# Kernel tuning notes

Measured on AMD Instinct MI355X. Metric: run time of the kernel, lower is better.

The kernel has to match this reference:

```python
import jax, jax.numpy as jnp
import numpy as np

N = 100_000      # nodes
E = 1_200_000    # edges (avg degree 12)
F_IN = 6         # node_features
H = 64           # hidden_channels
L = 3            # num_layers
EPS = 1e-5       # BatchNorm eps


def setup_inputs() -> dict:
    key = jax.random.key(0)
    ks = jax.random.split(key, 16)
    s = 0.1
    return {
        "x": jax.random.normal(ks[0], (N, F_IN), jnp.float32),
        "edge_index": jax.random.randint(ks[1], (2, E), 0, N, dtype=jnp.int32),
        "edge_attr": jax.random.uniform(ks[2], (E, 1), jnp.float32),
        # node encoder
        "W_enc": jax.random.normal(ks[3], (F_IN, H), jnp.float32) * s,
        "b_enc": jnp.zeros((H,), jnp.float32),
        # per-layer GNN params (stacked over L layers)
        "W_edge": jax.random.normal(ks[4], (L, 1, H), jnp.float32) * s,
        "b_edge": jnp.zeros((L, H), jnp.float32),
        "W_upd": jax.random.normal(ks[5], (L, 2 * H, H), jnp.float32) * s,
        "b_upd": jnp.zeros((L, H), jnp.float32),
        # batch norm (eval mode: running stats)
        "bn_gamma": jnp.ones((L, H), jnp.float32),
        "bn_beta": jnp.zeros((L, H), jnp.float32),
        "bn_mean": jnp.zeros((L, H), jnp.float32),
        "bn_var": jnp.ones((L, H), jnp.float32),
        # path predictor MLP
        "W_p1": jax.random.normal(ks[6], (H, H), jnp.float32) * s,
        "b_p1": jnp.zeros((H,), jnp.float32),
        "W_p2": jax.random.normal(ks[7], (H, 1), jnp.float32) * s,
        "b_p2": jnp.zeros((1,), jnp.float32),
    }


def reference(x, edge_index, edge_attr, W_enc, b_enc, W_edge, b_edge,
              W_upd, b_upd, bn_gamma, bn_beta, bn_mean, bn_var,
              W_p1, b_p1, W_p2, b_p2):
    src, dst = edge_index[0], edge_index[1]  # PyG source_to_target flow
    h = x @ W_enc + b_enc                    # [N, H]
    for i in range(L):
        # message: x_j * lin_edge(edge_attr)
        edge_feat = edge_attr @ W_edge[i] + b_edge[i]      # [E, H]
        msg = h[src] * edge_feat                           # gather + multiply
        # aggregate: scatter-max to target nodes; PyG fills empty rows with 0
        agg = jax.ops.segment_max(msg, dst, num_segments=N)
        agg = jnp.where(jnp.isfinite(agg), agg, 0.0)
        # update: relu(lin_update(cat[x, aggr]))
        h = jax.nn.relu(jnp.concatenate([h, agg], axis=1) @ W_upd[i] + b_upd[i])
        # BatchNorm1d (eval) + relu  (dropout p=0.1 is identity at inference)
        h = (h - bn_mean[i]) * (bn_gamma[i] / jnp.sqrt(bn_var[i] + EPS)) + bn_beta[i]
        h = jax.nn.relu(h)
    # path predictor: Linear -> ReLU -> Linear
    path_scores = jax.nn.relu(h @ W_p1 + b_p1) @ W_p2 + b_p2  # [N, 1]
    return path_scores
```

## Files before the change

### kernel.cpp

```cpp
#include <hip/hip_runtime.h>
#include <hip/hip_fp16.h>

#define FIN 6
#define HC 64
#define LAYERS 3
#define CAP 64

typedef _Float16 f16x8 __attribute__((ext_vector_type(8)));
typedef float f32x4 __attribute__((ext_vector_type(4)));

__global__ void PathfindingGNN_17274358464713_kernel() {}

__global__ __launch_bounds__(256) void k_enc_scatter(const float* __restrict__ x,
                                                     const float* __restrict__ Wenc,
                                                     const float* __restrict__ benc,
                                                     __half* __restrict__ h16,
                                                     int Nn,
                                                     const int* __restrict__ src,
                                                     const int* __restrict__ dst,
                                                     const float* __restrict__ ea,
                                                     int* __restrict__ counts,
                                                     unsigned int* __restrict__ bucket,
                                                     int E, int edgeB) {
  if ((int)blockIdx.x < edgeB) {
    int e = blockIdx.x * 256 + threadIdx.x;
    if (e < E) {
      int d = dst[e];
      int p = atomicAdd(&counts[d], 1);
      if (p < CAP) {
        unsigned int q = (unsigned int)(ea[e] * 32767.0f + 0.5f);
        bucket[d * CAP + p] = (unsigned int)src[e] | (q << 17);
      }
    }
    return;
  }
  int idx = (blockIdx.x - edgeB) * 256 + threadIdx.x;
  if (idx >= Nn * HC) return;
  int n = idx >> 6, c = idx & 63;
  float s = benc[c];
#pragma unroll
  for (int f = 0; f < FIN; ++f)
    s = fmaf(x[n * FIN + f], Wenc[f * HC + c], s);
  h16[idx] = __float2half(s);
}

__global__ __launch_bounds__(256, 6) void k_layer(const __half* __restrict__ h16,
                                                  const int* __restrict__ counts,
                                                  const unsigned int* __restrict__ bucket,
                                                  const float* __restrict__ We, const float* __restrict__ be,
                                                  const float* __restrict__ W, const float* __restrict__ b,
                                                  const float* __restrict__ gam, const float* __restrict__ bet,
                                                  const float* __restrict__ mean, const float* __restrict__ var,
                                                  __half* __restrict__ out16, int Nn,
                                                  int last, const float* __restrict__ Wp1,
                                                  const float* __restrict__ bp1, const float* __restrict__ Wp2,
                                                  const float* __restrict__ bp2, float* __restrict__ pred) {
  __shared__ alignas(16) __half Wt[64][136];
  __shared__ alignas(16) __half Asm[64][72];

  const int tid = threadIdx.x;
  const int nb = blockIdx.x * 64;
  const int w = tid >> 6;
  const float inv15 = 1.0f / 32767.0f;

  for (int i = tid; i < 128 * 64; i += 256) {
    int k = i >> 6, col = i & 63;
    Wt[col][k] = __float2half(W[i]);
  }

  {
    const int lhw = tid & 31;
    const int hw = (tid >> 5) & 1;
    const int ch0 = lhw * 2;
    const float2 wev = *(const float2*)&We[ch0];
    const float2 bev = *(const float2*)&be[ch0];
    for (int i = 0; i < 8; ++i) {
      int nl = w * 16 + i + 8 * hw;
      int nc = min(nb + nl, Nn - 1);
      int r = nc * CAP;
      int r1 = r + min(counts[nc], CAP);
      float m0 = -INFINITY, m1 = -INFINITY;
#define PROC(vv) {                                                                     \
      unsigned int v_ = (vv);                                                          \
      float qf = (float)(v_ >> 17) * inv15;                                            \
      float2 hf = __half22float2(*(const __half2*)&h16[(v_ & 0x1FFFFu) * HC + ch0]);   \
      m0 = fmaxf(m0, hf.x * fmaf(qf, wev.x, bev.x));                                   \
      m1 = fmaxf(m1, hf.y * fmaf(qf, wev.y, bev.y)); }
      for (; r + 8 <= r1; r += 8) {
        uint4 va = *(const uint4*)&bucket[r];
        uint4 vb = *(const uint4*)&bucket[r + 4];
        PROC(va.x) PROC(va.y) PROC(va.z) PROC(va.w)
        PROC(vb.x) PROC(vb.y) PROC(vb.z) PROC(vb.w)
      }
      if (r + 4 <= r1) {
        uint4 va = *(const uint4*)&bucket[r];
        PROC(va.x) PROC(va.y) PROC(va.z) PROC(va.w)
        r += 4;
      }
      for (; r < r1; ++r) { PROC(bucket[r]) }
#undef PROC
      float o0 = (m0 == -INFINITY) ? 0.0f : m0;
      float o1 = (m1 == -INFINITY) ? 0.0f : m1;
      *(__half2*)&Asm[nl][ch0] = __floats2half2_rn(o0, o1);
    }
  }
  __syncthreads();

  const int lr = tid & 15;
  const int lg = (tid >> 4) & 3;
  f32x4 acc[4];
#pragma unroll
  for (int t = 0; t < 4; ++t) acc[t] = (f32x4){0.f, 0.f, 0.f, 0.f};
  const int arow = min(nb + w * 16 + lr, Nn - 1);
#pragma unroll
  for (int kc = 0; kc < 4; ++kc) {
    const int kof = kc * 32 + lg * 8;
    f16x8 a;
    if (kc < 2)
      a = *(const f16x8*)&h16[arow * HC + kof];
    else
      a = *(const f16x8*)&Asm[w * 16 + lr][kof - 64];
#pragma unroll
    for (int t = 0; t < 4; ++t) {
      f16x8 bf = *(const f16x8*)&Wt[t * 16 + lr][kof];
      acc[t] = __builtin_amdgcn_mfma_f32_16x16x32_f16(a, bf, acc[t], 0, 0, 0);
    }
  }

  float o[4][4];
#pragma unroll
  for (int t = 0; t < 4; ++t) {
    int cc = t * 16 + lr;
    float bias = b[cc];
    float sc = gam[cc] * rsqrtf(var[cc] + 1e-5f);
    float sh = bet[cc] - mean[cc] * sc;
#pragma unroll
    for (int r = 0; r < 4; ++r) {
      float v = fmaxf(acc[t][r] + bias, 0.f);
      o[t][r] = fmaxf(fmaf(v, sc, sh), 0.f);
    }
  }

  const int rbase = nb + w * 16 + lg * 4;
  if (!last) {
#pragma unroll
    for (int r = 0; r < 4; ++r) {
      int n = rbase + r;
      if (n < Nn) {
#pragma unroll
        for (int t = 0; t < 4; ++t)
          out16[n * HC + t * 16 + lr] = __float2half(o[t][r]);
      }
    }
    return;
  }

  __syncthreads();
#pragma unroll
  for (int t = 0; t < 4; ++t)
#pragma unroll
    for (int r = 0; r < 4; ++r)
      Asm[w * 16 + lg * 4 + r][t * 16 + lr] = __float2half(o[t][r]);
  for (int i = tid; i < 64 * 64; i += 256) {
    int k = i >> 6, col = i & 63;
    Wt[col][k] = __float2half(Wp1[i]);
  }
  __syncthreads();

  f32x4 acc2[4];
#pragma unroll
  for (int t = 0; t < 4; ++t) acc2[t] = (f32x4){0.f, 0.f, 0.f, 0.f};
#pragma unroll
  for (int kc = 0; kc < 2; ++kc) {
    const int kof = kc * 32 + lg * 8;
    f16x8 a = *(const f16x8*)&Asm[w * 16 + lr][kof];
#pragma unroll
    for (int t = 0; t < 4; ++t) {
      f16x8 bf = *(const f16x8*)&Wt[t * 16 + lr][kof];
      acc2[t] = __builtin_amdgcn_mfma_f32_16x16x32_f16(a, bf, acc2[t], 0, 0, 0);
    }
  }

  float s[4] = {0.f, 0.f, 0.f, 0.f};
#pragma unroll
  for (int t = 0; t < 4; ++t) {
    int cc = t * 16 + lr;
    float b1 = bp1[cc], w2 = Wp2[cc];
#pragma unroll
    for (int r = 0; r < 4; ++r) {
      float pv = fmaxf(acc2[t][r] + b1, 0.f);
      s[r] = fmaf(pv, w2, s[r]);
    }
  }
#pragma unroll
  for (int msk = 1; msk < 16; msk <<= 1) {
#pragma unroll
    for (int r = 0; r < 4; ++r) s[r] += __shfl_xor(s[r], msk, 64);
  }
  if (lr == 0) {
    float b2 = bp2[0];
#pragma unroll
    for (int r = 0; r < 4; ++r) {
      int n = rbase + r;
      if (n < Nn) pred[n] = s[r] + b2;
    }
  }
}

extern "C" void kernel_launch(void* const* d_in, const int* in_sizes, int n_in,
                              void* d_out, int out_size, void* d_ws, size_t ws_size,
                              hipStream_t stream) {
  const float* x = (const float*)d_in[0];
  const int* eidx = (const int*)d_in[1];
  const float* eattr = (const float*)d_in[2];
  const float* Wenc = (const float*)d_in[3];
  const float* benc = (const float*)d_in[4];
  const float* Wedge = (const float*)d_in[5];
  const float* bedge = (const float*)d_in[6];
  const float* Wupd = (const float*)d_in[7];
  const float* bupd = (const float*)d_in[8];
  const float* bng = (const float*)d_in[9];
  const float* bnb = (const float*)d_in[10];
  const float* bnm = (const float*)d_in[11];
  const float* bnv = (const float*)d_in[12];
  const float* Wp1 = (const float*)d_in[13];
  const float* bp1 = (const float*)d_in[14];
  const float* Wp2 = (const float*)d_in[15];
  const float* bp2 = (const float*)d_in[16];

  const int Nn = in_sizes[0] / FIN;
  const int E = in_sizes[1] / 2;
  const int* src = eidx;
  const int* dst = eidx + E;
  const int NH = Nn * HC;

  size_t off = 0;
  char* base = (char*)d_ws;
  auto carve = [&](size_t bytes) -> void* {
    void* p = base + off;
    off += (bytes + 255) & ~(size_t)255;
    return p;
  };
  int* counts = (int*)carve((size_t)Nn * 4);
  unsigned int* bucket = (unsigned int*)carve((size_t)Nn * CAP * 4);
  __half* hA16 = (__half*)carve((size_t)NH * 2);
  __half* hB16 = (__half*)carve((size_t)NH * 2);
  if (off > ws_size) return;

  int nhB = (NH + 255) / 256;
  int edgeB = (E + 255) / 256;
  int updB = (Nn + 63) / 64;

  hipMemsetAsync(counts, 0, (size_t)Nn * 4, stream);
  k_enc_scatter<<<edgeB + nhB, 256, 0, stream>>>(x, Wenc, benc, hA16, Nn,
                                                 src, dst, eattr, counts, bucket, E, edgeB);

  __half* hc16 = hA16;
  __half* hn16 = hB16;
  for (int i = 0; i < LAYERS; ++i) {
    int last = (i == LAYERS - 1) ? 1 : 0;
    k_layer<<<updB, 256, 0, stream>>>(hc16, counts, bucket,
                                      Wedge + i * HC, bedge + i * HC,
                                      Wupd + i * 2 * HC * HC, bupd + i * HC,
                                      bng + i * HC, bnb + i * HC, bnm + i * HC, bnv + i * HC,
                                      hn16, Nn,
                                      last, Wp1, bp1, Wp2, bp2, (float*)d_out);
    __half* t16 = hc16; hc16 = hn16; hn16 = t16;
  }
}
```

Baseline: 365.4 us.

## Prefetch edge buckets with nontemporal loads and vectorize encoder writes

Bucket records are now written and read with nontemporal hints, so edge lists streamed once per layer do not evict the reused node features from cache. The gather loop software-prefetches the first four records of the next node while the current one is processed. Per-node counts are loaded once per wave and broadcast with shuffles. The encoder computes two channels per thread with half2 stores. The cost is more branching in the aggregation loop and a narrower unrolled body (4 records instead of 8 per step), which may reduce memory-level parallelism for high-degree nodes.

```diff
diff --git a/kernel.cpp b/kernel.cpp
--- a/kernel.cpp
+++ b/kernel.cpp
@@ -8,6 +8,11 @@
 
 typedef _Float16 f16x8 __attribute__((ext_vector_type(8)));
 typedef float f32x4 __attribute__((ext_vector_type(4)));
+typedef unsigned int u32x4 __attribute__((ext_vector_type(4)));
+
+__device__ inline u32x4 ntload4(const unsigned int* p) {
+  return __builtin_nontemporal_load(reinterpret_cast<const u32x4*>(p));
+}
 
 __global__ void PathfindingGNN_17274358464713_kernel() {}
 
@@ -29,19 +34,24 @@
       int p = atomicAdd(&counts[d], 1);
       if (p < CAP) {
         unsigned int q = (unsigned int)(ea[e] * 32767.0f + 0.5f);
-        bucket[d * CAP + p] = (unsigned int)src[e] | (q << 17);
+        unsigned int rec = (unsigned int)src[e] | (q << 17);
+        __builtin_nontemporal_store(rec, &bucket[d * CAP + p]);
       }
     }
     return;
   }
   int idx = (blockIdx.x - edgeB) * 256 + threadIdx.x;
-  if (idx >= Nn * HC) return;
-  int n = idx >> 6, c = idx & 63;
-  float s = benc[c];
-#pragma unroll
-  for (int f = 0; f < FIN; ++f)
-    s = fmaf(x[n * FIN + f], Wenc[f * HC + c], s);
-  h16[idx] = __float2half(s);
+  if (idx >= Nn * (HC / 2)) return;
+  int n = idx >> 5, cp = (idx & 31) * 2;
+  float s0 = benc[cp], s1 = benc[cp + 1];
+#pragma unroll
+  for (int f = 0; f < FIN; ++f) {
+    float xv = x[n * FIN + f];
+    float2 wv = *(const float2*)&Wenc[f * HC + cp];
+    s0 = fmaf(xv, wv.x, s0);
+    s1 = fmaf(xv, wv.y, s1);
+  }
+  *(__half2*)&h16[n * HC + cp] = __floats2half2_rn(s0, s1);
 }
 
 __global__ __launch_bounds__(256, 6) void k_layer(const __half* __restrict__ h16,
@@ -74,11 +84,19 @@
     const int ch0 = lhw * 2;
     const float2 wev = *(const float2*)&We[ch0];
     const float2 bev = *(const float2*)&be[ch0];
+    int ldn = min(nb + w * 16 + (tid & 15), Nn - 1);
+    int ldc = min(counts[ldn], CAP);
+    auto rof = [&](int i) {
+      return min(nb + w * 16 + i + 8 * hw, Nn - 1) * CAP;
+    };
+    u32x4 pf = ntload4(&bucket[rof(0)]);
     for (int i = 0; i < 8; ++i) {
       int nl = w * 16 + i + 8 * hw;
-      int nc = min(nb + nl, Nn - 1);
-      int r = nc * CAP;
-      int r1 = r + min(counts[nc], CAP);
+      int cnt = __shfl(ldc, i + 8 * hw, 64);
+      int r0 = rof(i);
+      int r1 = r0 + cnt;
+      u32x4 cur = pf;
+      if (i < 7) pf = ntload4(&bucket[rof(i + 1)]);
       float m0 = -INFINITY, m1 = -INFINITY;
 #define PROC(vv) {                                                                     \
       unsigned int v_ = (vv);                                                          \
@@ -86,18 +104,21 @@
       float2 hf = __half22float2(*(const __half2*)&h16[(v_ & 0x1FFFFu) * HC + ch0]);   \
       m0 = fmaxf(m0, hf.x * fmaf(qf, wev.x, bev.x));                                   \
       m1 = fmaxf(m1, hf.y * fmaf(qf, wev.y, bev.y)); }
-      for (; r + 8 <= r1; r += 8) {
-        uint4 va = *(const uint4*)&bucket[r];
-        uint4 vb = *(const uint4*)&bucket[r + 4];
+      if (cnt > 0) {
+        PROC(cur.x)
+        if (cnt > 1) PROC(cur.y)
+        if (cnt > 2) PROC(cur.z)
+        if (cnt > 3) PROC(cur.w)
+      }
+      int r = r0 + 4;
+      for (; r + 4 <= r1; r += 4) {
+        u32x4 va = ntload4(&bucket[r]);
         PROC(va.x) PROC(va.y) PROC(va.z) PROC(va.w)
-        PROC(vb.x) PROC(vb.y) PROC(vb.z) PROC(vb.w)
-      }
-      if (r + 4 <= r1) {
-        uint4 va = *(const uint4*)&bucket[r];
-        PROC(va.x) PROC(va.y) PROC(va.z) PROC(va.w)
-        r += 4;
-      }
-      for (; r < r1; ++r) { PROC(bucket[r]) }
+      }
+      for (; r < r1; ++r) {
+        unsigned int v = __builtin_nontemporal_load(&bucket[r]);
+        PROC(v)
+      }
 #undef PROC
       float o0 = (m0 == -INFINITY) ? 0.0f : m0;
       float o1 = (m1 == -INFINITY) ? 0.0f : m1;
@@ -247,7 +268,7 @@
   __half* hB16 = (__half*)carve((size_t)NH * 2);
   if (off > ws_size) return;
 
-  int nhB = (NH + 255) / 256;
+  int nhB = (Nn * (HC / 2) + 255) / 256;
   int edgeB = (E + 255) / 256;
   int updB = (Nn + 63) / 64;
 
```

Result: slower. 456.6 us (+25.0%).
